# Optimization experiments

Measured on AMD Instinct MI355X. Metric: run time of the kernel, lower is better.

The kernel has to match this reference:

```python
import jax, jax.numpy as jnp
import numpy as np

B, S, H = 2, 1024, 2048
D = 256          # index_dimension = min(index.embedding_dimension, hidden_size)
R = 32           # LoRA rank
K = 4            # index_k neighbors per query token
N_DB = 100000    # rows in the external index


def setup_inputs() -> dict:
    key = jax.random.key(0)
    ks = jax.random.split(key, 7)
    return {
        "hidden_states": jax.random.normal(ks[0], (B, S, H), jnp.float32),
        "db_keys": jax.random.normal(ks[1], (N_DB, D), jnp.float32),
        "db_values": jax.random.normal(ks[2], (N_DB, D), jnp.float32),
        "wq_in": jax.random.normal(ks[3], (H, R), jnp.float32) * 0.02,
        "wq_out": jax.random.normal(ks[4], (R, D), jnp.float32) * 0.02,
        "wv_in": jax.random.normal(ks[5], (D, R), jnp.float32) * 0.02,
        "wv_out": jax.random.normal(ks[6], (R, H), jnp.float32) * 0.02,
    }


def reference(hidden_states, db_keys, db_values, wq_in, wq_out, wv_in, wv_out):
    b, s, h = hidden_states.shape
    d = wq_out.shape[1]
    # query LoRA projection: hidden -> r -> index_dim
    q = (hidden_states @ wq_in) @ wq_out            # [B, S, D]

    # external k-NN lookup (exact L2 top-k over index table), no_grad in torch
    qf = q.reshape(b * s, d)                        # [B*S, D]
    qn = jnp.sum(qf * qf, axis=-1, keepdims=True)   # [B*S, 1]
    kn = jnp.sum(db_keys * db_keys, axis=-1)        # [N_DB]
    dist = qn - 2.0 * (qf @ db_keys.T) + kn[None, :]  # [B*S, N_DB]
    _, idx = jax.lax.top_k(-dist, K)                # [B*S, K] nearest neighbors

    # gather KV and reshape to [B, S*K, D] (matches torch view calls)
    kv_key = jax.lax.stop_gradient(db_keys[idx]).reshape(b, s * K, d)
    kv_val = jax.lax.stop_gradient(db_values[idx]).reshape(b, s * K, d)

    # SDPA, is_causal=True with Lq != Lk: top-left aligned tril mask (j <= i)
    scale = 1.0 / np.sqrt(d).astype(np.float32)
    scores = jnp.einsum('bqd,bkd->bqk', q, kv_key) * scale  # [B, S, S*K]
    mask = jnp.arange(s * K)[None, :] <= jnp.arange(s)[:, None]
    scores = jnp.where(mask[None, :, :], scores, jnp.finfo(scores.dtype).min)
    attn = jax.nn.softmax(scores, axis=-1)
    out = jnp.einsum('bqk,bkd->bqd', attn, kv_val)  # [B, S, D]

    # value LoRA projection: index_dim -> r -> hidden
    return (out @ wv_in) @ wv_out                   # [B, S, H]
```

## Files before the change

kernel.cpp:

```cpp
#include <hip/hip_runtime.h>
#include <cfloat>

#define B_   2
#define S_   1024
#define H_   2048
#define D_   256
#define R_   32
#define K_   4
#define NDB_ 100000

#define TSEL 256
#define NSEL (B_ * TSEL)

#define NCHUNK     61
#define CHUNK_ROWS 1664
#define TILES      13
#define NT         128
#define MT         64
#define KC         64
#define LSTR       68

#define NEG_INF  (-3.0e38f)
#define IDX_MAX  0x7fffffff

#define OFF_Q     0
#define OFF_KN    0x200000
#define OFF_PS    0x280000
#define OFF_PI    0x300000
#define OFF_IDX   0x380000
#define OFF_CAND  0x3A0000
#define OFF_KVT   0x400000
#define OFF_AO    0x600000
#define OFF_KVV   0x800000
#define OFF_DBK16 0xA00000

typedef unsigned short ushort_t;
typedef unsigned int   uint_t;
typedef __attribute__((ext_vector_type(8)))  __bf16 bf16x8;
typedef __attribute__((ext_vector_type(16))) float  f32x16;

__device__ __forceinline__ void ins4(float sc, int n, float s[4], int id[4]) {
  if (sc > s[3] || (sc == s[3] && n < id[3])) {
    s[3] = sc; id[3] = n;
#pragma unroll
    for (int k = 3; k > 0; --k) {
      if (s[k] > s[k - 1] || (s[k] == s[k - 1] && id[k] < id[k - 1])) {
        float ts = s[k]; s[k] = s[k - 1]; s[k - 1] = ts;
        int ti = id[k]; id[k] = id[k - 1]; id[k - 1] = ti;
      }
    }
  }
}

__device__ __forceinline__ uint_t bfpack(float a, float b) {
  uint_t ua = __float_as_uint(a), ub = __float_as_uint(b);
  ua = (ua + 0x7fffu + ((ua >> 16) & 1u)) >> 16;
  ub = (ub + 0x7fffu + ((ub >> 16) & 1u)) >> 16;
  return ua | (ub << 16);
}

__global__ __launch_bounds__(256) void k_compute_q(
    const float* __restrict__ hidden, const float* __restrict__ wq_in,
    const float* __restrict__ wq_out, float* __restrict__ q) {
  __shared__ float hrow[H_];
  __shared__ float part[8][R_];
  __shared__ float q1[R_];
  const int m = blockIdx.x;
  const int t = threadIdx.x;
  const float* hp = hidden + (size_t)m * H_;
  ((float4*)hrow)[t]       = ((const float4*)hp)[t];
  ((float4*)hrow)[t + 256] = ((const float4*)hp)[t + 256];
  __syncthreads();
  const int r = t & 31, c = t >> 5;
  float p = 0.f;
#pragma unroll 4
  for (int e = c * 256; e < c * 256 + 256; ++e)
    p = fmaf(hrow[e], wq_in[(size_t)e * R_ + r], p);
  part[c][r] = p;
  __syncthreads();
  if (t < R_) {
    float s = 0.f;
#pragma unroll
    for (int cc = 0; cc < 8; ++cc) s += part[cc][t];
    q1[t] = s;
  }
  __syncthreads();
  float acc = 0.f;
#pragma unroll
  for (int rr = 0; rr < R_; ++rr) acc = fmaf(q1[rr], wq_out[rr * D_ + t], acc);
  q[(size_t)m * D_ + t] = acc;
}

__global__ __launch_bounds__(256) void k_kn_cvt(const float* __restrict__ dbk,
                                               float* __restrict__ kn,
                                               ushort_t* __restrict__ dbk16) {
  const int w = threadIdx.x >> 6, l = threadIdx.x & 63;
  const int n = blockIdx.x * 4 + w;
  if (n >= NDB_) return;
  const float4 v = ((const float4*)(dbk + (size_t)n * D_))[l];
  uint2 p; p.x = bfpack(v.x, v.y); p.y = bfpack(v.z, v.w);
  ((uint2*)(dbk16 + (size_t)n * D_))[l] = p;
  float s = v.x * v.x + v.y * v.y + v.z * v.z + v.w * v.w;
#pragma unroll
  for (int off = 32; off; off >>= 1) s += __shfl_down(s, off);
  if (l == 0) kn[n] = s;
}

__global__ __launch_bounds__(256) void k_kn(const float* __restrict__ dbk,
                                            float* __restrict__ kn) {
  const int w = threadIdx.x >> 6, l = threadIdx.x & 63;
  const int n = blockIdx.x * 4 + w;
  if (n >= NDB_) return;
  const float4 v = ((const float4*)(dbk + (size_t)n * D_))[l];
  float s = v.x * v.x + v.y * v.y + v.z * v.z + v.w * v.w;
#pragma unroll
  for (int off = 32; off; off >>= 1) s += __shfl_down(s, off);
  if (l == 0) kn[n] = s;
}

__global__ __launch_bounds__(256, 2) void k_knn_mfma(
    const float* __restrict__ q, const ushort_t* __restrict__ dbk16,
    const float* __restrict__ kn, float* __restrict__ pscore,
    int* __restrict__ pidx) {
  __shared__ __align__(16) char smem[65536];
  ushort_t* sA = (ushort_t*)smem;
  ushort_t* sB = (ushort_t*)(smem + 32768);
  float*    sS = (float*)(smem + 32768);

  const int tid = threadIdx.x;
  const int wv = tid >> 6, ln = tid & 63;
  const int lm = ln & 31, lh = ln >> 5;
  const int tx = tid & 15, ty = tid >> 4;
  const int qb = blockIdx.x, chunk = blockIdx.y;
  const int row_base = chunk * CHUNK_ROWS;

  {
    const int m = tid & 63, cg = tid >> 6;
    const int sq = qb * MT + m;
    const float* qp = q + ((size_t)((sq >> 8) * S_ + (sq & 255))) * D_;
#pragma unroll
    for (int cc = 0; cc < 8; ++cc) {
      const int c = cg * 8 + cc;
      const float4 v0 = *(const float4*)(qp + c * 8);
      const float4 v1 = *(const float4*)(qp + c * 8 + 4);
      uint4 pk;
      pk.x = bfpack(v0.x, v0.y); pk.y = bfpack(v0.z, v0.w);
      pk.z = bfpack(v1.x, v1.y); pk.w = bfpack(v1.z, v1.w);
      *(uint4*)&sA[(m * 32 + (c ^ (m & 7))) * 8] = pk;
    }
  }

  float s4[4][4]; int i4[4][4];
#pragma unroll
  for (int a = 0; a < 4; ++a)
#pragma unroll
    for (int b = 0; b < 4; ++b) { s4[a][b] = NEG_INF; i4[a][b] = IDX_MAX; }

  for (int tile = 0; tile < TILES; ++tile) {
    const int row0 = row_base + tile * NT;
    if (row0 >= NDB_) break;

    f32x16 acc0, acc1;
#pragma unroll
    for (int r = 0; r < 16; ++r) { acc0[r] = 0.f; acc1[r] = 0.f; }

    for (int kh = 0; kh < 2; ++kh) {
      __syncthreads();
      {
        const int n_in = ln >> 4;
        const int p    = ln & 15;
#pragma unroll
        for (int i = 0; i < 8; ++i) {
          const int nloc = wv * 32 + i * 4 + n_in;
          int krow = row0 + nloc; if (krow >= NDB_) krow = NDB_ - 1;
          const int c = p ^ (nloc & 7);
          const ushort_t* gp = dbk16 + (size_t)krow * D_ + (kh * 16 + c) * 8;
          ushort_t* lp = sB + (size_t)(wv * 32 + i * 4) * 128;
          __builtin_amdgcn_global_load_lds(
              (const __attribute__((address_space(1))) void*)gp,
              (__attribute__((address_space(3))) void*)lp, 16, 0, 0);
        }
      }
      __syncthreads();
      const int nB = wv * 32 + lm;
      const int bswz = nB & 7;
#pragma unroll
      for (int ks = 0; ks < 8; ++ks) {
        const int cA = kh * 16 + ks * 2 + lh;
        const bf16x8 a0 = *(const bf16x8*)&sA[(lm * 32 + (cA ^ (lm & 7))) * 8];
        const bf16x8 a1 = *(const bf16x8*)&sA[((32 + lm) * 32 + (cA ^ (lm & 7))) * 8];
        const bf16x8 bb = *(const bf16x8*)&sB[(nB * 16 + ((ks * 2 + lh) ^ bswz)) * 8];
        acc0 = __builtin_amdgcn_mfma_f32_32x32x16_bf16(a0, bb, acc0, 0, 0, 0);
        acc1 = __builtin_amdgcn_mfma_f32_32x32x16_bf16(a1, bb, acc1, 0, 0, 0);
      }
    }
    __syncthreads();

    {
      const int n = (tid >> 6) * 32 + lm;
#pragma unroll
      for (int r = 0; r < 16; ++r) {
        const int mrow = (r & 3) + 8 * (r >> 2) + 4 * lh;
        sS[mrow * 128 + n]        = acc0[r];
        sS[(32 + mrow) * 128 + n] = acc1[r];
      }
    }
    __syncthreads();

    {
      const int nbase = row0 + tx * 8;
      float knv[8]; int nok[8];
#pragma unroll
      for (int j = 0; j < 8; ++j) {
        nok[j] = (nbase + j < NDB_);
        knv[j] = nok[j] ? kn[nbase + j] : 0.f;
      }
#pragma unroll
      for (int qi = 0; qi < 4; ++qi) {
        const int m = ty * 4 + qi;
        const float4 v0 = *(const float4*)&sS[m * 128 + tx * 8];
        const float4 v1 = *(const float4*)&sS[m * 128 + tx * 8 + 4];
        const float sv[8] = {v0.x, v0.y, v0.z, v0.w, v1.x, v1.y, v1.z, v1.w};
        float v[8];
#pragma unroll
        for (int j = 0; j < 8; ++j)
          v[j] = nok[j] ? fmaf(2.f, sv[j], -knv[j]) : NEG_INF;
        const float mx = fmaxf(fmaxf(fmaxf(v[0], v[1]), fmaxf(v[2], v[3])),
                               fmaxf(fmaxf(v[4], v[5]), fmaxf(v[6], v[7])));
        if (mx >= s4[qi][3]) {
#pragma unroll
          for (int j = 0; j < 8; ++j)
            if (nok[j]) ins4(v[j], nbase + j, s4[qi], i4[qi]);
        }
      }
    }
  }

  __syncthreads();
  float* cs = (float*)smem;
  int*   ci = (int*)(smem + 64 * 65 * 4);
#pragma unroll
  for (int qi = 0; qi < 4; ++qi)
#pragma unroll
    for (int k = 0; k < 4; ++k) {
      cs[(ty * 4 + qi) * 65 + tx * 4 + k] = s4[qi][k];
      ci[(ty * 4 + qi) * 65 + tx * 4 + k] = i4[qi][k];
    }
  __syncthreads();
  if (tid < 64) {
    float fs[4]; int fi[4];
#pragma unroll
    for (int k = 0; k < 4; ++k) { fs[k] = NEG_INF; fi[k] = IDX_MAX; }
    for (int c = 0; c < 64; ++c)
      ins4(cs[tid * 65 + c], ci[tid * 65 + c], fs, fi);
    const int sq = qb * MT + tid;
    float* po = pscore + ((size_t)sq * NCHUNK + chunk) * 4;
    int*   io = pidx   + ((size_t)sq * NCHUNK + chunk) * 4;
#pragma unroll
    for (int k = 0; k < 4; ++k) { po[k] = fs[k]; io[k] = fi[k]; }
  }
}

__global__ __launch_bounds__(256) void k_knn_partial(
    const float* __restrict__ q, const float* __restrict__ dbk,
    const float* __restrict__ kn, float* __restrict__ pscore,
    int* __restrict__ pidx) {
  __shared__ float smem[3 * KC * LSTR];
  float* sA  = smem;
  float* sB0 = smem + KC * LSTR;
  float* sB1 = smem + 2 * KC * LSTR;
  const int tid = threadIdx.x;
  const int tx = tid & 15, ty = tid >> 4;
  const int chunk = blockIdx.x, qb = blockIdx.y;
  const int arq = tid >> 2;
  const int aqd = (tid & 3) * 4;
  const int brk = tid >> 1;
  const int bh  = tid & 1;
  const int bcol = ((brk >> 3) << 2) | (brk & 3);
  float* sBw = (brk & 4) ? sB1 : sB0;
  const int sq_a = qb * MT + arq;
  const float* qsrc = q + ((size_t)((sq_a >> 8) * S_ + (sq_a & 255))) * D_;
  float s4[4][4]; int i4[4][4];
#pragma unroll
  for (int a = 0; a < 4; ++a)
#pragma unroll
    for (int b = 0; b < 4; ++b) { s4[a][b] = NEG_INF; i4[a][b] = IDX_MAX; }
  const int row_base = chunk * CHUNK_ROWS;
  for (int tile = 0; tile < TILES; ++tile) {
    const int row0 = row_base + tile * NT;
    if (row0 >= NDB_) break;
    int krow = row0 + brk; if (krow >= NDB_) krow = NDB_ - 1;
    const float* ksrc = dbk + (size_t)krow * D_;
    float acc[4][8];
#pragma unroll
    for (int a = 0; a < 4; ++a)
#pragma unroll
      for (int b = 0; b < 8; ++b) acc[a][b] = 0.f;
    for (int kc = 0; kc < 4; ++kc) {
      __syncthreads();
#pragma unroll
      for (int p = 0; p < 4; ++p) {
        const int kkl = p * 16 + aqd;
        const float4 v = *(const float4*)(qsrc + kc * KC + kkl);
        sA[(kkl + 0) * LSTR + arq] = v.x;
        sA[(kkl + 1) * LSTR + arq] = v.y;
        sA[(kkl + 2) * LSTR + arq] = v.z;
        sA[(kkl + 3) * LSTR + arq] = v.w;
      }
#pragma unroll
      for (int p = 0; p < 8; ++p) {
        const int kkl = bh * 32 + p * 4;
        const float4 v = *(const float4*)(ksrc + kc * KC + kkl);
        sBw[(kkl + 0) * LSTR + bcol] = v.x;
        sBw[(kkl + 1) * LSTR + bcol] = v.y;
        sBw[(kkl + 2) * LSTR + bcol] = v.z;
        sBw[(kkl + 3) * LSTR + bcol] = v.w;
      }
      __syncthreads();
#pragma unroll 4
      for (int kk = 0; kk < KC; ++kk) {
        const float4 a  = *(const float4*)&sA [kk * LSTR + ty * 4];
        const float4 b0 = *(const float4*)&sB0[kk * LSTR + tx * 4];
        const float4 b1 = *(const float4*)&sB1[kk * LSTR + tx * 4];
        const float av[4] = {a.x, a.y, a.z, a.w};
        const float bv[8] = {b0.x, b0.y, b0.z, b0.w, b1.x, b1.y, b1.z, b1.w};
#pragma unroll
        for (int qi = 0; qi < 4; ++qi)
#pragma unroll
          for (int nj = 0; nj < 8; ++nj)
            acc[qi][nj] = fmaf(av[qi], bv[nj], acc[qi][nj]);
      }
    }
#pragma unroll
    for (int nj = 0; nj < 8; ++nj) {
      const int n = row0 + tx * 8 + nj;
      if (n < NDB_) {
        const float knj = kn[n];
        ins4(2.f * acc[0][nj] - knj, n, s4[0], i4[0]);
        ins4(2.f * acc[1][nj] - knj, n, s4[1], i4[1]);
        ins4(2.f * acc[2][nj] - knj, n, s4[2], i4[2]);
        ins4(2.f * acc[3][nj] - knj, n, s4[3], i4[3]);
      }
    }
  }
  __syncthreads();
  float* cs = smem;
  int*   ci = (int*)(smem + 64 * 65);
#pragma unroll
  for (int qi = 0; qi < 4; ++qi)
#pragma unroll
    for (int k = 0; k < 4; ++k) {
      cs[(ty * 4 + qi) * 65 + tx * 4 + k] = s4[qi][k];
      ci[(ty * 4 + qi) * 65 + tx * 4 + k] = i4[qi][k];
    }
  __syncthreads();
  if (tid < 64) {
    float fs[4]; int fi[4];
#pragma unroll
    for (int k = 0; k < 4; ++k) { fs[k] = NEG_INF; fi[k] = IDX_MAX; }
    for (int c = 0; c < 64; ++c)
      ins4(cs[tid * 65 + c], ci[tid * 65 + c], fs, fi);
    const int sq = qb * MT + tid;
    float* po = pscore + ((size_t)sq * NCHUNK + chunk) * 4;
    int*   io = pidx   + ((size_t)sq * NCHUNK + chunk) * 4;
#pragma unroll
    for (int k = 0; k < 4; ++k) { po[k] = fs[k]; io[k] = fi[k]; }
  }
}

template <int RANKS>
__device__ __forceinline__ void merge_top(const float* __restrict__ pscore,
                                          const int* __restrict__ pidx,
                                          int* __restrict__ outp) {
  const int sq = blockIdx.x, l = threadIdx.x;
  float s4[4]; int i4[4];
#pragma unroll
  for (int k = 0; k < 4; ++k) { s4[k] = NEG_INF; i4[k] = IDX_MAX; }
  for (int c = l; c < NCHUNK * 4; c += 64)
    ins4(pscore[(size_t)sq * NCHUNK * 4 + c], pidx[(size_t)sq * NCHUNK * 4 + c], s4, i4);
#pragma unroll
  for (int r = 0; r < RANKS; ++r) {
    float s = s4[0]; int i = i4[0];
#pragma unroll
    for (int off = 32; off; off >>= 1) {
      float so = __shfl_down(s, off); int io = __shfl_down(i, off);
      if (so > s || (so == s && io < i)) { s = so; i = io; }
    }
    const float sw = __shfl(s, 0); const int iw = __shfl(i, 0);
    if (l == 0) outp[sq * RANKS + r] = iw;
    if (s4[0] == sw && i4[0] == iw) {
      s4[0] = s4[1]; i4[0] = i4[1];
      s4[1] = s4[2]; i4[1] = i4[2];
      s4[2] = s4[3]; i4[2] = i4[3];
      s4[3] = NEG_INF; i4[3] = IDX_MAX;
    }
  }
}

__global__ __launch_bounds__(64) void k_knn_merge4(const float* __restrict__ ps,
                                                   const int* __restrict__ pi,
                                                   int* __restrict__ knn_idx) {
  merge_top<4>(ps, pi, knn_idx);
}
__global__ __launch_bounds__(64) void k_knn_merge16(const float* __restrict__ ps,
                                                    const int* __restrict__ pi,
                                                    int* __restrict__ cand) {
  merge_top<16>(ps, pi, cand);
}

__global__ __launch_bounds__(256) void k_rescore(const float* __restrict__ q,
                                                 const float* __restrict__ dbk,
                                                 const float* __restrict__ kn,
                                                 const int* __restrict__ cand,
                                                 int* __restrict__ knn_idx) {
  __shared__ float scs[16];
  __shared__ int   sci[16];
  const int sq = blockIdx.x, wv = threadIdx.x >> 6, l = threadIdx.x & 63;
  const float* qp = q + ((size_t)((sq >> 8) * S_ + (sq & 255))) * D_;
  const float4 qv = ((const float4*)qp)[l];
  for (int cc = wv; cc < 16; cc += 4) {
    const int n = cand[sq * 16 + cc];
    const float4 kv = ((const float4*)(dbk + (size_t)n * D_))[l];
    float s = qv.x * kv.x + qv.y * kv.y + qv.z * kv.z + qv.w * kv.w;
#pragma unroll
    for (int off = 32; off; off >>= 1) s += __shfl_down(s, off);
    if (l == 0) { scs[cc] = 2.f * s - kn[n]; sci[cc] = n; }
  }
  __syncthreads();
  if (threadIdx.x == 0) {
    float s4[4]; int i4[4];
#pragma unroll
    for (int k = 0; k < 4; ++k) { s4[k] = NEG_INF; i4[k] = IDX_MAX; }
#pragma unroll
    for (int c = 0; c < 16; ++c) ins4(scs[c], sci[c], s4, i4);
#pragma unroll
    for (int k = 0; k < 4; ++k) knn_idx[sq * 4 + k] = i4[k];
  }
}

__global__ __launch_bounds__(256) void k_gather(const float* __restrict__ dbk,
                                                const float* __restrict__ dbv,
                                                const int* __restrict__ knn_idx,
                                                float* __restrict__ kvT,
                                                float* __restrict__ kvV) {
  const int b = blockIdx.x >> 6, j0 = (blockIdx.x & 63) * 16;
  const int w = threadIdx.x >> 6, l = threadIdx.x & 63;
  float* dstT = kvT + (size_t)b * D_ * 1024;
  float* dstV = kvV + (size_t)b * 1024 * D_;
  for (int jj = w; jj < 16; jj += 4) {
    const int j = j0 + jj;
    const int row = knn_idx[b * 1024 + j];
    const float4 kv = ((const float4*)(dbk + (size_t)row * D_))[l];
    dstT[(4 * l + 0) * 1024 + j] = kv.x;
    dstT[(4 * l + 1) * 1024 + j] = kv.y;
    dstT[(4 * l + 2) * 1024 + j] = kv.z;
    dstT[(4 * l + 3) * 1024 + j] = kv.w;
    const float4 vv = ((const float4*)(dbv + (size_t)row * D_))[l];
    ((float4*)(dstV + (size_t)j * D_))[l] = vv;
  }
}

__global__ __launch_bounds__(256) void k_attn(const float* __restrict__ qarr,
                                              const float* __restrict__ kvT,
                                              const float* __restrict__ kvV,
                                              float* __restrict__ attout) {
  __shared__ float qrow[D_];
  __shared__ float attw[1024];
  __shared__ float red1[4], red2[4];
  const int b = blockIdx.x >> 10, i = blockIdx.x & 1023;
  const int t = threadIdx.x;
  const int nk = i + 1;
  qrow[t] = qarr[((size_t)b * S_ + i) * D_ + t];
  __syncthreads();
  const int cmax = (nk + 255) >> 8;
  const float scale = 0.0625f;
  float sc[4]; float mloc = NEG_INF;
#pragma unroll
  for (int c = 0; c < 4; ++c) {
    sc[c] = NEG_INF;
    if (c < cmax) {
      const int j = c * 256 + t;
      float a = 0.f;
      const float* kp = kvT + (size_t)b * D_ * 1024 + j;
#pragma unroll 8
      for (int d = 0; d < D_; ++d) a = fmaf(qrow[d], kp[(size_t)d * 1024], a);
      if (j < nk) sc[c] = a * scale;
    }
    mloc = fmaxf(mloc, sc[c]);
  }
#pragma unroll
  for (int off = 32; off; off >>= 1) mloc = fmaxf(mloc, __shfl_down(mloc, off));
  if ((t & 63) == 0) red1[t >> 6] = mloc;
  __syncthreads();
  const float mmax = fmaxf(fmaxf(red1[0], red1[1]), fmaxf(red1[2], red1[3]));
  float sloc = 0.f; float pv[4];
#pragma unroll
  for (int c = 0; c < 4; ++c) {
    pv[c] = (sc[c] > NEG_INF * 0.5f) ? __expf(sc[c] - mmax) : 0.f;
    sloc += pv[c];
  }
#pragma unroll
  for (int off = 32; off; off >>= 1) sloc += __shfl_down(sloc, off);
  if ((t & 63) == 0) red2[t >> 6] = sloc;
  __syncthreads();
  const float inv = 1.f / (red2[0] + red2[1] + red2[2] + red2[3]);
#pragma unroll
  for (int c = 0; c < 4; ++c)
    if (c < cmax) attw[c * 256 + t] = pv[c] * inv;
  __syncthreads();
  const float* vb = kvV + (size_t)b * 1024 * D_;
  float a0 = 0.f, a1 = 0.f, a2 = 0.f, a3 = 0.f;
  int j = 0;
  for (; j + 4 <= nk; j += 4) {
    a0 = fmaf(attw[j + 0], vb[(size_t)(j + 0) * D_ + t], a0);
    a1 = fmaf(attw[j + 1], vb[(size_t)(j + 1) * D_ + t], a1);
    a2 = fmaf(attw[j + 2], vb[(size_t)(j + 2) * D_ + t], a2);
    a3 = fmaf(attw[j + 3], vb[(size_t)(j + 3) * D_ + t], a3);
  }
  for (; j < nk; ++j) a0 = fmaf(attw[j], vb[(size_t)j * D_ + t], a0);
  attout[((size_t)b * S_ + i) * D_ + t] = (a0 + a1) + (a2 + a3);
}

__global__ __launch_bounds__(256) void k_out(const float* __restrict__ attout,
                                             const float* __restrict__ wv_in,
                                             const float* __restrict__ wv_out,
                                             float* __restrict__ y) {
  __shared__ float row[D_];
  __shared__ float part[8][R_];
  __shared__ float t32[R_];
  const int m = blockIdx.x, t = threadIdx.x;
  row[t] = attout[(size_t)m * D_ + t];
  __syncthreads();
  const int r = t & 31, c = t >> 5;
  float p = 0.f;
#pragma unroll
  for (int d = c * 32; d < c * 32 + 32; ++d)
    p = fmaf(row[d], wv_in[d * R_ + r], p);
  part[c][r] = p;
  __syncthreads();
  if (t < R_) {
    float s = 0.f;
#pragma unroll
    for (int cc = 0; cc < 8; ++cc) s += part[cc][t];
    t32[t] = s;
  }
  __syncthreads();
  for (int hh = t; hh < H_; hh += 256) {
    float a = 0.f;
#pragma unroll
    for (int rr = 0; rr < R_; ++rr) a = fmaf(t32[rr], wv_out[rr * H_ + hh], a);
    y[(size_t)m * H_ + hh] = a;
  }
}

extern "C" void kernel_launch(void* const* d_in, const int* in_sizes, int n_in,
                              void* d_out, int out_size, void* d_ws, size_t ws_size,
                              hipStream_t stream) {
  const float* hidden  = (const float*)d_in[0];
  const float* db_keys = (const float*)d_in[1];
  const float* db_vals = (const float*)d_in[2];
  const float* wq_in   = (const float*)d_in[3];
  const float* wq_out  = (const float*)d_in[4];
  const float* wv_in   = (const float*)d_in[5];
  const float* wv_out  = (const float*)d_in[6];
  float* out = (float*)d_out;

  char* ws = (char*)d_ws;
  float*    q      = (float*)(ws + OFF_Q);
  float*    kn     = (float*)(ws + OFF_KN);
  float*    ps     = (float*)(ws + OFF_PS);
  int*      pi     = (int*)  (ws + OFF_PI);
  int*      idx    = (int*)  (ws + OFF_IDX);
  int*      cand   = (int*)  (ws + OFF_CAND);
  float*    kvT    = (float*)(ws + OFF_KVT);
  float*    attout = (float*)(ws + OFF_AO);
  float*    kvV    = (float*)(ws + OFF_KVV);
  ushort_t* dbk16  = (ushort_t*)(ws + OFF_DBK16);

  const size_t need = (size_t)OFF_DBK16 + (size_t)NDB_ * D_ * 2;

  k_compute_q<<<B_ * S_, 256, 0, stream>>>(hidden, wq_in, wq_out, q);
  if (ws_size >= need) {
    k_kn_cvt<<<(NDB_ + 3) / 4, 256, 0, stream>>>(db_keys, kn, dbk16);
    k_knn_mfma<<<dim3(8, NCHUNK), 256, 0, stream>>>(q, dbk16, kn, ps, pi);
    k_knn_merge16<<<NSEL, 64, 0, stream>>>(ps, pi, cand);
    k_rescore<<<NSEL, 256, 0, stream>>>(q, db_keys, kn, cand, idx);
  } else {
    k_kn<<<(NDB_ + 3) / 4, 256, 0, stream>>>(db_keys, kn);
    k_knn_partial<<<dim3(NCHUNK, 8), 256, 0, stream>>>(q, db_keys, kn, ps, pi);
    k_knn_merge4<<<NSEL, 64, 0, stream>>>(ps, pi, idx);
  }
  k_gather<<<2 * 64, 256, 0, stream>>>(db_keys, db_vals, idx, kvT, kvV);
  k_attn<<<B_ * S_, 256, 0, stream>>>(q, kvT, kvV, attout);
  k_out<<<B_ * S_, 256, 0, stream>>>(attout, wv_in, wv_out, out);
}
```

Baseline: 544.0 us.

## Tile attention over four queries per block and remap knn grid order

The attention kernel now handles four query rows per block. Each loaded K and V element is reused across four dot products, the scale is folded into q, and query groups are interleaved from both ends of the sequence so causal work is spread evenly across blocks. The knn MFMA kernel switches to a flattened 1D grid that puts adjacent chunks for the same query block next to each other, with padding blocks that exit early. The cost is more registers and shared memory per attention block and only 512 attention blocks, so there is less parallelism.

```diff
diff --git a/kernel.cpp b/kernel.cpp
--- a/kernel.cpp
+++ b/kernel.cpp
@@ -22,6 +22,8 @@
 
 #define NEG_INF  (-3.0e38f)
 #define IDX_MAX  0x7fffffff
+
+#define TQ 4
 
 #define OFF_Q     0
 #define OFF_KN    0x200000
@@ -127,11 +129,15 @@
   ushort_t* sB = (ushort_t*)(smem + 32768);
   float*    sS = (float*)(smem + 32768);
 
+  const int fid = blockIdx.x;
+  const int chunk = (fid & 7) + 8 * ((fid >> 3) & 7);
+  const int qb = fid >> 6;
+  if (chunk >= NCHUNK) return;
+
   const int tid = threadIdx.x;
   const int wv = tid >> 6, ln = tid & 63;
   const int lm = ln & 31, lh = ln >> 5;
   const int tx = tid & 15, ty = tid >> 4;
-  const int qb = blockIdx.x, chunk = blockIdx.y;
   const int row_base = chunk * CHUNK_ROWS;
 
   {
@@ -460,65 +466,144 @@
   }
 }
 
+template <int CMAX>
+__device__ __forceinline__ void qk_dots(const float* __restrict__ kb, int t,
+                                        const float (*qrow)[D_], float a[4][TQ]) {
+#pragma unroll 2
+  for (int d = 0; d < D_; d += 4) {
+    float qv[TQ][4];
+#pragma unroll
+    for (int q = 0; q < TQ; ++q) {
+      const float4 v = *(const float4*)&qrow[q][d];
+      qv[q][0] = v.x; qv[q][1] = v.y; qv[q][2] = v.z; qv[q][3] = v.w;
+    }
+#pragma unroll
+    for (int dd = 0; dd < 4; ++dd) {
+      float kv[CMAX];
+#pragma unroll
+      for (int c = 0; c < CMAX; ++c)
+        kv[c] = kb[(size_t)(d + dd) * 1024 + c * 256 + t];
+#pragma unroll
+      for (int c = 0; c < CMAX; ++c)
+#pragma unroll
+        for (int q = 0; q < TQ; ++q)
+          a[c][q] = fmaf(qv[q][dd], kv[c], a[c][q]);
+    }
+  }
+}
+
 __global__ __launch_bounds__(256) void k_attn(const float* __restrict__ qarr,
                                               const float* __restrict__ kvT,
                                               const float* __restrict__ kvV,
                                               float* __restrict__ attout) {
-  __shared__ float qrow[D_];
-  __shared__ float attw[1024];
-  __shared__ float red1[4], red2[4];
-  const int b = blockIdx.x >> 10, i = blockIdx.x & 1023;
+  __shared__ float qrow[TQ][D_];
+  __shared__ float attw[TQ][1024];
+  __shared__ float pvred[4][TQ][D_];
+  __shared__ float redm[4][TQ], reds[4][TQ];
+
+  const int fid = blockIdx.x;
+  const int b = fid & 1;
+  const int g = fid >> 1;
+  const int h = g >> 1;
+  const int grp = (g & 1) ? (255 - h) : h;
+  const int i0 = grp * TQ;
   const int t = threadIdx.x;
-  const int nk = i + 1;
-  qrow[t] = qarr[((size_t)b * S_ + i) * D_ + t];
-  __syncthreads();
-  const int cmax = (nk + 255) >> 8;
-  const float scale = 0.0625f;
-  float sc[4]; float mloc = NEG_INF;
-#pragma unroll
-  for (int c = 0; c < 4; ++c) {
-    sc[c] = NEG_INF;
-    if (c < cmax) {
-      const int j = c * 256 + t;
-      float a = 0.f;
-      const float* kp = kvT + (size_t)b * D_ * 1024 + j;
-#pragma unroll 8
-      for (int d = 0; d < D_; ++d) a = fmaf(qrow[d], kp[(size_t)d * 1024], a);
-      if (j < nk) sc[c] = a * scale;
-    }
-    mloc = fmaxf(mloc, sc[c]);
-  }
-#pragma unroll
-  for (int off = 32; off; off >>= 1) mloc = fmaxf(mloc, __shfl_down(mloc, off));
-  if ((t & 63) == 0) red1[t >> 6] = mloc;
-  __syncthreads();
-  const float mmax = fmaxf(fmaxf(red1[0], red1[1]), fmaxf(red1[2], red1[3]));
-  float sloc = 0.f; float pv[4];
-#pragma unroll
-  for (int c = 0; c < 4; ++c) {
-    pv[c] = (sc[c] > NEG_INF * 0.5f) ? __expf(sc[c] - mmax) : 0.f;
-    sloc += pv[c];
-  }
-#pragma unroll
-  for (int off = 32; off; off >>= 1) sloc += __shfl_down(sloc, off);
-  if ((t & 63) == 0) red2[t >> 6] = sloc;
-  __syncthreads();
-  const float inv = 1.f / (red2[0] + red2[1] + red2[2] + red2[3]);
+  const int w = t >> 6, l = t & 63;
+  const int nkmax = i0 + TQ;
+  const int cmax = (nkmax + 255) >> 8;
+
+  {
+    const float4 v = ((const float4*)(qarr + ((size_t)b * S_ + i0 + w) * D_))[l];
+    float4 sv;
+    sv.x = v.x * 0.0625f; sv.y = v.y * 0.0625f;
+    sv.z = v.z * 0.0625f; sv.w = v.w * 0.0625f;
+    ((float4*)&qrow[w][0])[l] = sv;
+  }
+  __syncthreads();
+
+  const float* kb = kvT + (size_t)b * D_ * 1024;
+  float a[4][TQ];
 #pragma unroll
   for (int c = 0; c < 4; ++c)
-    if (c < cmax) attw[c * 256 + t] = pv[c] * inv;
-  __syncthreads();
+#pragma unroll
+    for (int q = 0; q < TQ; ++q) a[c][q] = 0.f;
+  switch (cmax) {
+    case 1: qk_dots<1>(kb, t, qrow, a); break;
+    case 2: qk_dots<2>(kb, t, qrow, a); break;
+    case 3: qk_dots<3>(kb, t, qrow, a); break;
+    default: qk_dots<4>(kb, t, qrow, a); break;
+  }
+#pragma unroll
+  for (int c = 0; c < 4; ++c)
+    if (c < cmax)
+#pragma unroll
+      for (int q = 0; q < TQ; ++q)
+        if (c * 256 + t > i0 + q) a[c][q] = NEG_INF;
+
+  float M[TQ];
+#pragma unroll
+  for (int q = 0; q < TQ; ++q) {
+    float m = NEG_INF;
+    for (int c = 0; c < cmax; ++c) m = fmaxf(m, a[c][q]);
+#pragma unroll
+    for (int off = 32; off; off >>= 1) m = fmaxf(m, __shfl_down(m, off));
+    if (l == 0) redm[w][q] = m;
+  }
+  __syncthreads();
+#pragma unroll
+  for (int q = 0; q < TQ; ++q)
+    M[q] = fmaxf(fmaxf(redm[0][q], redm[1][q]), fmaxf(redm[2][q], redm[3][q]));
+  float inv[TQ];
+#pragma unroll
+  for (int q = 0; q < TQ; ++q) {
+    float s = 0.f;
+    for (int c = 0; c < cmax; ++c) {
+      const float p = (a[c][q] > 0.5f * NEG_INF) ? __expf(a[c][q] - M[q]) : 0.f;
+      a[c][q] = p; s += p;
+    }
+#pragma unroll
+    for (int off = 32; off; off >>= 1) s += __shfl_down(s, off);
+    if (l == 0) reds[w][q] = s;
+  }
+  __syncthreads();
+#pragma unroll
+  for (int q = 0; q < TQ; ++q)
+    inv[q] = 1.f / (reds[0][q] + reds[1][q] + reds[2][q] + reds[3][q]);
+  for (int c = 0; c < cmax; ++c)
+#pragma unroll
+    for (int q = 0; q < TQ; ++q)
+      attw[q][c * 256 + t] = a[c][q] * inv[q];
+  __syncthreads();
+
   const float* vb = kvV + (size_t)b * 1024 * D_;
-  float a0 = 0.f, a1 = 0.f, a2 = 0.f, a3 = 0.f;
-  int j = 0;
-  for (; j + 4 <= nk; j += 4) {
-    a0 = fmaf(attw[j + 0], vb[(size_t)(j + 0) * D_ + t], a0);
-    a1 = fmaf(attw[j + 1], vb[(size_t)(j + 1) * D_ + t], a1);
-    a2 = fmaf(attw[j + 2], vb[(size_t)(j + 2) * D_ + t], a2);
-    a3 = fmaf(attw[j + 3], vb[(size_t)(j + 3) * D_ + t], a3);
-  }
-  for (; j < nk; ++j) a0 = fmaf(attw[j], vb[(size_t)j * D_ + t], a0);
-  attout[((size_t)b * S_ + i) * D_ + t] = (a0 + a1) + (a2 + a3);
+  float4 acc[TQ];
+#pragma unroll
+  for (int q = 0; q < TQ; ++q) acc[q] = make_float4(0.f, 0.f, 0.f, 0.f);
+#pragma unroll 2
+  for (int j = w; j < nkmax; j += 4) {
+    const float4 v = ((const float4*)(vb + (size_t)j * D_))[l];
+#pragma unroll
+    for (int q = 0; q < TQ; ++q) {
+      const float p = attw[q][j];
+      acc[q].x = fmaf(p, v.x, acc[q].x);
+      acc[q].y = fmaf(p, v.y, acc[q].y);
+      acc[q].z = fmaf(p, v.z, acc[q].z);
+      acc[q].w = fmaf(p, v.w, acc[q].w);
+    }
+  }
+#pragma unroll
+  for (int q = 0; q < TQ; ++q) ((float4*)&pvred[w][q][0])[l] = acc[q];
+  __syncthreads();
+  {
+    const int q = t >> 6;
+    float4 s = make_float4(0.f, 0.f, 0.f, 0.f);
+#pragma unroll
+    for (int ww = 0; ww < 4; ++ww) {
+      const float4 p = ((const float4*)&pvred[ww][q][0])[l];
+      s.x += p.x; s.y += p.y; s.z += p.z; s.w += p.w;
+    }
+    ((float4*)(attout + ((size_t)b * S_ + i0 + q) * D_))[l] = s;
+  }
 }
 
 __global__ __launch_bounds__(256) void k_out(const float* __restrict__ attout,
@@ -582,7 +667,7 @@
   k_compute_q<<<B_ * S_, 256, 0, stream>>>(hidden, wq_in, wq_out, q);
   if (ws_size >= need) {
     k_kn_cvt<<<(NDB_ + 3) / 4, 256, 0, stream>>>(db_keys, kn, dbk16);
-    k_knn_mfma<<<dim3(8, NCHUNK), 256, 0, stream>>>(q, dbk16, kn, ps, pi);
+    k_knn_mfma<<<512, 256, 0, stream>>>(q, dbk16, kn, ps, pi);
     k_knn_merge16<<<NSEL, 64, 0, stream>>>(ps, pi, cand);
     k_rescore<<<NSEL, 256, 0, stream>>>(q, db_keys, kn, cand, idx);
   } else {
@@ -591,6 +676,6 @@
     k_knn_merge4<<<NSEL, 64, 0, stream>>>(ps, pi, idx);
   }
   k_gather<<<2 * 64, 256, 0, stream>>>(db_keys, db_vals, idx, kvT, kvV);
-  k_attn<<<B_ * S_, 256, 0, stream>>>(q, kvT, kvV, attout);
+  k_attn<<<512, 256, 0, stream>>>(q, kvT, kvV, attout);
   k_out<<<B_ * S_, 256, 0, stream>>>(attout, wv_in, wv_out, out);
 }
```

Measured after the change: 495.7 us. 1.1x faster.
